# Optimization experiments

Measured on AMD Instinct MI355X. Metric: run time of the kernel, lower is better.

Reference implementation:

```python
import jax, jax.numpy as jnp
import numpy as np

N, E, G = 50000, 800000, 64
NODE_DIM, HID, HEADS, EDGE_DIM = 128, 256, 4, 2
LAYER_IN = [NODE_DIM, HID, HID]
LAYER_HEADS = [HEADS, HEADS, 1]
BN_EPS = 1e-5


def setup_inputs() -> dict:
    key = jax.random.key(0)
    ks = iter(jax.random.split(key, 80))
    def nrm(shape, s=0.05):
        return jax.random.normal(next(ks), shape, jnp.float32) * s
    inp = {}
    inp['x'] = jax.random.normal(next(ks), (N, NODE_DIM), jnp.float32)
    inp['edge_index'] = jax.random.randint(next(ks), (2, E), 0, N, jnp.int32)
    inp['edge_attr'] = jax.random.normal(next(ks), (E, EDGE_DIM), jnp.float32)
    inp['batch'] = jnp.sort(jax.random.randint(next(ks), (N,), 0, G, jnp.int32))
    for i in range(3):
        H = LAYER_HEADS[i]; C = HID // H
        inp[f'W{i}'] = nrm((LAYER_IN[i], H * C))
        inp[f'asrc{i}'] = nrm((H, C))
        inp[f'adst{i}'] = nrm((H, C))
        inp[f'We{i}'] = nrm((EDGE_DIM, H * C))
        inp[f'aedge{i}'] = nrm((H, C))
        inp[f'bconv{i}'] = jnp.zeros((HID,), jnp.float32)
        inp[f'bn{i}_g'] = jnp.ones((HID,), jnp.float32)
        inp[f'bn{i}_b'] = jnp.zeros((HID,), jnp.float32)
        inp[f'bn{i}_m'] = nrm((HID,), 0.01)
        inp[f'bn{i}_v'] = jnp.ones((HID,), jnp.float32)
    inp['Wskip'] = nrm((NODE_DIM, HID))
    inp['bskip'] = jnp.zeros((HID,), jnp.float32)
    inp['Wp1'] = nrm((2 * HID, HID))
    inp['bp1'] = jnp.zeros((HID,), jnp.float32)
    inp['Wp2'] = nrm((HID, 1))
    inp['bp2'] = jnp.zeros((1,), jnp.float32)
    return inp


def gat_conv(x, src, dst, ea, W, a_s, a_d, We, a_e, b, H, concat):
    n = x.shape[0]
    C = W.shape[1] // H
    h = (x @ W).reshape(n, H, C)                      # [N,H,C]
    # attention logits per edge (src/dst node terms + edge term)
    al = ((h * a_s).sum(-1)[src]
          + (h * a_d).sum(-1)[dst]
          + ((ea @ We).reshape(-1, H, C) * a_e).sum(-1))  # [Et,H]
    al = jax.nn.leaky_relu(al, 0.2)
    # segment softmax over destination nodes
    amax = jax.ops.segment_max(al, dst, num_segments=n)
    ex = jnp.exp(al - amax[dst])
    den = jax.ops.segment_sum(ex, dst, num_segments=n)
    alpha = ex / (den[dst] + 1e-16)
    out = jax.ops.segment_sum(h[src] * alpha[..., None], dst, num_segments=n)  # [N,H,C]
    out = out.reshape(n, H * C) if concat else out.mean(axis=1)
    return out + b


def _forward(x, edge_index, edge_attr, batch, layer_params, Wskip, bskip, Wp1, bp1, Wp2, bp2):
    n = x.shape[0]
    # add self-loops (PyG GATConv default), edge_attr filled with mean
    loop = jnp.arange(n, dtype=edge_index.dtype)
    src = jnp.concatenate([edge_index[0], loop])
    dst = jnp.concatenate([edge_index[1], loop])
    ea = jnp.concatenate([edge_attr, jnp.broadcast_to(edge_attr.mean(0), (n, edge_attr.shape[1]))], axis=0)
    identity = x
    for i, (W, a_s, a_d, We, a_e, b, g, be, rm, rv) in enumerate(layer_params):
        layer_identity = (identity @ Wskip + bskip) if i == 0 else identity
        concat = i < 2
        H = LAYER_HEADS[i]
        h = gat_conv(x, src, dst, ea, W, a_s, a_d, We, a_e, b, H, concat)
        h = (h - rm) * jax.lax.rsqrt(rv + BN_EPS) * g + be   # BatchNorm1d (eval)
        h = jax.nn.elu(h)
        x = h + layer_identity
        identity = x
    # global mean + max pool per graph
    counts = jnp.maximum(jax.ops.segment_sum(jnp.ones((n,), x.dtype), batch, num_segments=G), 1.0)
    mean_pool = jax.ops.segment_sum(x, batch, num_segments=G) / counts[:, None]
    max_pool = jax.ops.segment_max(x, batch, num_segments=G)
    emb = jnp.concatenate([mean_pool, max_pool], axis=1)      # [G, 2*HID]
    hmid = jax.nn.relu(emb @ Wp1 + bp1)
    return hmid @ Wp2 + bp2                                   # [G, 1]


def reference(x, edge_index, edge_attr, batch,
              W0, asrc0, adst0, We0, aedge0, bconv0, bn0_g, bn0_b, bn0_m, bn0_v,
              W1, asrc1, adst1, We1, aedge1, bconv1, bn1_g, bn1_b, bn1_m, bn1_v,
              W2, asrc2, adst2, We2, aedge2, bconv2, bn2_g, bn2_b, bn2_m, bn2_v,
              Wskip, bskip, Wp1, bp1, Wp2, bp2):
    layer_params = [
        (W0, asrc0, adst0, We0, aedge0, bconv0, bn0_g, bn0_b, bn0_m, bn0_v),
        (W1, asrc1, adst1, We1, aedge1, bconv1, bn1_g, bn1_b, bn1_m, bn1_v),
        (W2, asrc2, adst2, We2, aedge2, bconv2, bn2_g, bn2_b, bn2_m, bn2_v),
    ]
    return _forward(x, edge_index, edge_attr, batch, layer_params, Wskip, bskip, Wp1, bp1, Wp2, bp2)
```

## Files before the change

### kernel.cpp

```cpp
#include <hip/hip_runtime.h>
#include <cfloat>

#define Nn 50000
#define Ee 800000
#define Etot (Ee + Nn)
#define Gg 64
#define HIDc 256
#define BN_EPS 1e-5f

typedef unsigned int   uint32;
typedef unsigned short ushort16;
typedef short  bf16x8 __attribute__((ext_vector_type(8)));
typedef float  f32x4  __attribute__((ext_vector_type(4)));

__device__ inline ushort16 f2bf(float f) {
    uint32 u = __float_as_uint(f);
    u = (u + 0x7fffu + ((u >> 16) & 1u)) >> 16;
    return (ushort16)u;
}
__device__ inline uint32 pack2(float a, float b) {
    return (uint32)f2bf(a) | ((uint32)f2bf(b) << 16);
}
__device__ inline uint32 fenc(float f) {
    uint32 b = __float_as_uint(f);
    return (b & 0x80000000u) ? ~b : (b | 0x80000000u);
}
__device__ inline float fdec(uint32 u) {
    uint32 b = (u & 0x80000000u) ? (u & 0x7fffffffu) : ~u;
    return __uint_as_float(b);
}

__device__ inline long ws_index(int c, int k, int KB) {
    int cb = c >> 4, m = c & 15, kb = k >> 5, q = (k >> 3) & 3, e = k & 7;
    return (((long)(cb * KB + kb) * 64 + q * 16 + m) << 3) + e;
}

#define CVT4 (Nn * 128 / 4)
#define CVT_BLKS ((CVT4 + 255) / 256)
#define EBKS ((Etot + 255) / 256)
__global__ __launch_bounds__(256) void prep_kernel(
        const float* __restrict__ ea, float* __restrict__ ea_s,
        const float* __restrict__ We0, const float* __restrict__ ae0,
        const float* __restrict__ We1, const float* __restrict__ ae1,
        const float* __restrict__ We2, const float* __restrict__ ae2,
        float* __restrict__ M,
        const float* __restrict__ W0, const float* __restrict__ Wskip,
        const float* __restrict__ W1, const float* __restrict__ W2,
        ushort16* __restrict__ WtC, ushort16* __restrict__ Wt1,
        ushort16* __restrict__ Wt2,
        const float* __restrict__ x, ushort16* __restrict__ xbf,
        const int* __restrict__ ei, int* __restrict__ counts,
        const float* __restrict__ bc0, const float* __restrict__ g0,
        const float* __restrict__ b0, const float* __restrict__ m0,
        const float* __restrict__ v0,
        const float* __restrict__ bc1, const float* __restrict__ g1,
        const float* __restrict__ b1, const float* __restrict__ m1,
        const float* __restrict__ v1,
        const float* __restrict__ bc2, const float* __restrict__ g2,
        const float* __restrict__ b2, const float* __restrict__ m2,
        const float* __restrict__ v2,
        float* __restrict__ bnf) {
    int bid = blockIdx.x, t = threadIdx.x;
    if (bid < 256) {
        __shared__ float sh0[256], sh1[256];
        float s0 = 0.f, s1 = 0.f;
        for (int e = bid * 256 + t; e < Ee; e += 256 * 256) {
            s0 += ea[2 * e];
            s1 += ea[2 * e + 1];
        }
        sh0[t] = s0; sh1[t] = s1;
        __syncthreads();
        for (int off = 128; off > 0; off >>= 1) {
            if (t < off) { sh0[t] += sh0[t + off]; sh1[t] += sh1[t + off]; }
            __syncthreads();
        }
        if (t == 0) { atomicAdd(&ea_s[0], sh0[0]); atomicAdd(&ea_s[1], sh1[0]); }
    } else if (bid == 256) {
        if (t >= 18) return;
        int l = t < 8 ? 0 : (t < 16 ? 1 : 2);
        int r = t - l * 8;
        const float* We = (l == 0) ? We0 : (l == 1 ? We1 : We2);
        const float* ae = (l == 0) ? ae0 : (l == 1 ? ae1 : ae2);
        int Hl = (l < 2) ? 4 : 1;
        int Cl = 256 / Hl;
        int d = r / Hl, hh = r % Hl;
        float s = 0.f;
        for (int c = 0; c < Cl; ++c)
            s += We[d * 256 + hh * Cl + c] * ae[hh * Cl + c];
        M[l * 8 + r] = s;
    } else if (bid < 385) {
        int k = bid - 257;
        WtC[ws_index(t, k, 4)] = f2bf(W0[(long)k * 256 + t]);
    } else if (bid < 513) {
        int k = bid - 385;
        WtC[ws_index(256 + t, k, 4)] = f2bf(Wskip[(long)k * 256 + t]);
    } else if (bid < 769) {
        int k = bid - 513;
        Wt1[ws_index(t, k, 8)] = f2bf(W1[(long)k * 256 + t]);
    } else if (bid < 1025) {
        int k = bid - 769;
        Wt2[ws_index(t, k, 8)] = f2bf(W2[(long)k * 256 + t]);
    } else if (bid == 1025) {
        for (int ll = 0; ll < 3; ++ll) {
            const float* bc = ll == 0 ? bc0 : (ll == 1 ? bc1 : bc2);
            const float* gg = ll == 0 ? g0  : (ll == 1 ? g1  : g2);
            const float* bb = ll == 0 ? b0  : (ll == 1 ? b1  : b2);
            const float* mm = ll == 0 ? m0  : (ll == 1 ? m1  : m2);
            const float* vv = ll == 0 ? v0  : (ll == 1 ? v1  : v2);
            float s = gg[t] * rsqrtf(vv[t] + BN_EPS);
            bnf[ll * 512 + t]       = s;
            bnf[ll * 512 + 256 + t] = (bc[t] - mm[t]) * s + bb[t];
        }
    } else if (bid < 1026 + CVT_BLKS) {
        int i = (bid - 1026) * 256 + t;
        if (i < CVT4) {
            float4 v = *(const float4*)&x[i * 4];
            ushort4 o;
            o.x = f2bf(v.x); o.y = f2bf(v.y); o.z = f2bf(v.z); o.w = f2bf(v.w);
            *(ushort4*)&xbf[i * 4] = o;
        }
    } else {
        int e = (bid - 1026 - CVT_BLKS) * 256 + t;
        if (e < Etot) {
            int d = (e < Ee) ? ei[Ee + e] : (e - Ee);
            atomicAdd(&counts[d], 1);
        }
    }
}

__global__ void scan1_kernel(const int* __restrict__ in, int* __restrict__ inc,
                             int* __restrict__ bsums) {
    __shared__ int sh[256];
    int i = blockIdx.x * 256 + threadIdx.x;
    int v = (i < Nn) ? in[i] : 0;
    sh[threadIdx.x] = v;
    __syncthreads();
    for (int off = 1; off < 256; off <<= 1) {
        int t = ((int)threadIdx.x >= off) ? sh[threadIdx.x - off] : 0;
        __syncthreads();
        sh[threadIdx.x] += t;
        __syncthreads();
    }
    if (i < Nn) inc[i] = sh[threadIdx.x];
    if (threadIdx.x == 255) bsums[blockIdx.x] = sh[255];
}

__global__ void scan23_kernel(const int* __restrict__ inc, const int* __restrict__ bsums,
                              int* __restrict__ row_start, int* __restrict__ cursor, int nb) {
    __shared__ int sh[256];
    int b = blockIdx.x, t = threadIdx.x;
    sh[t] = (t < b && t < nb) ? bsums[t] : 0;
    __syncthreads();
    for (int off = 128; off > 0; off >>= 1) {
        if (t < off) sh[t] += sh[t + off];
        __syncthreads();
    }
    int base = sh[0];
    int i = b * 256 + t;
    if (i < Nn) {
        int v = inc[i] + base;
        row_start[i + 1] = v;
        cursor[i + 1] = v;
    }
    if (i == 0) { row_start[0] = 0; cursor[0] = 0; }
}

__global__ void scatter_kernel(const int* __restrict__ ei, const float* __restrict__ ea,
                               const float* __restrict__ ea_sum, int* __restrict__ cursor,
                               int* __restrict__ src_sorted, float* __restrict__ ea_sorted) {
    int e = blockIdx.x * blockDim.x + threadIdx.x;
    if (e >= Etot) return;
    int s, d; float e0, e1;
    if (e < Ee) {
        s = ei[e]; d = ei[Ee + e];
        e0 = ea[2 * e]; e1 = ea[2 * e + 1];
    } else {
        s = d = e - Ee;
        const float invE = 1.f / (float)Ee;
        e0 = ea_sum[0] * invE; e1 = ea_sum[1] * invE;
    }
    int pos = atomicAdd(&cursor[d], 1);
    src_sorted[pos] = s;
    ea_sorted[2 * pos]     = e0;
    ea_sorted[2 * pos + 1] = e1;
}

#define LDK 40
__global__ __launch_bounds__(256) void mfma_gemm_kernel(
        const ushort16* __restrict__ A,
        const ushort16* __restrict__ WS,
        uint32* __restrict__ outF,
        uint32* __restrict__ outS,
        const float* __restrict__ bskip,
        const float* __restrict__ a_s, const float* __restrict__ a_d,
        float* __restrict__ ssrc, float* __restrict__ sdst,
        int n, int K) {
    __shared__ ushort16 As[128 * LDK];
    const int t    = threadIdx.x;
    const int row0 = blockIdx.x * 128;
    const int c0   = blockIdx.y * 128;
    const bool isSkip = (outS != nullptr) && (c0 >= 256);
    const int cc0  = isSkip ? c0 - 256 : c0;
    const int wave = t >> 6, lane = t & 63;
    const int wr = wave >> 1, wc = wave & 1;
    const int l15 = lane & 15, quad = lane >> 4;
    const int KB = K >> 5;

    f32x4 acc[4][4];
#pragma unroll
    for (int j = 0; j < 4; ++j)
#pragma unroll
        for (int i = 0; i < 4; ++i) {
            acc[j][i][0] = 0.f; acc[j][i][1] = 0.f;
            acc[j][i][2] = 0.f; acc[j][i][3] = 0.f;
        }

    const int sm = t & 127;
    const int so = t >> 7;

    for (int k0 = 0; k0 < K; k0 += 32) {
        const int kb = k0 >> 5;
#pragma unroll
        for (int h = 0; h < 2; ++h) {
            int oct = so + 2 * h;
            int grow = row0 + sm;
            uint4 va = make_uint4(0, 0, 0, 0);
            if (grow < n) va = *(const uint4*)&A[(long)grow * K + k0 + 8 * oct];
            *(uint4*)&As[sm * LDK + 8 * oct] = va;
        }
        bf16x8 bfv[4];
#pragma unroll
        for (int j = 0; j < 4; ++j) {
            int cb = ((c0 + wc * 64) >> 4) + j;
            bfv[j] = *(const bf16x8*)&WS[(((long)cb * KB + kb) * 64 + lane) << 3];
        }
        __syncthreads();
        bf16x8 af[4];
#pragma unroll
        for (int i = 0; i < 4; ++i)
            af[i] = *(const bf16x8*)&As[(wr * 64 + i * 16 + l15) * LDK + quad * 8];
#pragma unroll
        for (int j = 0; j < 4; ++j)
#pragma unroll
            for (int i = 0; i < 4; ++i)
                acc[j][i] = __builtin_amdgcn_mfma_f32_16x16x32_bf16(
                    bfv[j], af[i], acc[j][i], 0, 0, 0);
        __syncthreads();
    }

    float4 bb[4];
#pragma unroll
    for (int j = 0; j < 4; ++j) {
        if (isSkip) bb[j] = *(const float4*)&bskip[cc0 + wc * 64 + j * 16 + quad * 4];
        else        bb[j] = make_float4(0.f, 0.f, 0.f, 0.f);
    }

    uint32* tgt = isSkip ? outS : outF;
#pragma unroll
    for (int i = 0; i < 4; ++i) {
        int row = row0 + wr * 64 + i * 16 + l15;
        if (row >= n) continue;
#pragma unroll
        for (int j = 0; j < 4; ++j) {
            int col = cc0 + wc * 64 + j * 16 + quad * 4;
            uint2 pk;
            pk.x = pack2(acc[j][i][0] + bb[j].x, acc[j][i][1] + bb[j].y);
            pk.y = pack2(acc[j][i][2] + bb[j].z, acc[j][i][3] + bb[j].w);
            *(uint2*)&tgt[(long)row * 128 + (col >> 1)] = pk;
        }
    }

    if (!isSkip && a_s != nullptr) {
        float4 asv[4], adv[4];
#pragma unroll
        for (int j = 0; j < 4; ++j) {
            int col = cc0 + wc * 64 + j * 16 + quad * 4;
            asv[j] = *(const float4*)&a_s[col];
            adv[j] = *(const float4*)&a_d[col];
        }
        const int part = (cc0 + wc * 64) >> 6;
#pragma unroll
        for (int i = 0; i < 4; ++i) {
            float ps = 0.f, pd = 0.f;
#pragma unroll
            for (int j = 0; j < 4; ++j) {
                ps += acc[j][i][0] * asv[j].x + acc[j][i][1] * asv[j].y
                    + acc[j][i][2] * asv[j].z + acc[j][i][3] * asv[j].w;
                pd += acc[j][i][0] * adv[j].x + acc[j][i][1] * adv[j].y
                    + acc[j][i][2] * adv[j].z + acc[j][i][3] * adv[j].w;
            }
            ps += __shfl_xor(ps, 16); ps += __shfl_xor(ps, 32);
            pd += __shfl_xor(pd, 16); pd += __shfl_xor(pd, 32);
            if (quad == 0) {
                int row = row0 + wr * 64 + i * 16 + l15;
                if (row < n) {
                    ssrc[row * 4 + part] = ps;
                    sdst[row * 4 + part] = pd;
                }
            }
        }
    }
}

template <int H>
__global__ __launch_bounds__(256) void agg_fused_kernel(
        const int* __restrict__ src_sorted, const int* __restrict__ row_start,
        const float* __restrict__ ea_sorted, const float* __restrict__ ssrc,
        const float* __restrict__ sdst, const float* __restrict__ M,
        const uint32* __restrict__ hbuf2,
        const float* __restrict__ bnS, const float* __restrict__ bnB,
        const uint32* __restrict__ identity2, uint32* __restrict__ out2) {
    __shared__ int   s_sh[4][64];
    __shared__ float w_sh[4][64 * H];
    const int wv = threadIdx.x >> 6;
    const int l  = threadIdx.x & 63;
    const int node = blockIdx.x * 4 + wv;
    if (node >= Nn) return;
    const int hh = (H == 4) ? (l >> 4) : 0;
    const int beg = row_start[node], end = row_start[node + 1];

    const int c = 4 * l;
    const float4 scv = *(const float4*)&bnS[c];
    const float4 sbv = *(const float4*)&bnB[c];
    const uint2  idu = *(const uint2*)&identity2[(long)node * 128 + 2 * l];

    float M0[H], M1[H], sd[H];
    {
        float4 sdv = *(const float4*)&sdst[node * 4];
        if (H == 4) { sd[0] = sdv.x; sd[1] = sdv.y; sd[2] = sdv.z; sd[3] = sdv.w; }
        else         sd[0] = sdv.x + sdv.y + sdv.z + sdv.w;
#pragma unroll
        for (int h = 0; h < H; ++h) { M0[h] = M[h]; M1[h] = M[H + h]; }
    }

    float a0 = 0.f, a1 = 0.f, a2 = 0.f, a3 = 0.f, dnl = 0.f;
    const uint32 loff = (uint32)l << 3;

    for (int cb = beg; cb < end; cb += 64) {
        const int  el  = cb + l;
        const bool act = el < end;
        const int  elc = min(el, end - 1);
        const int  s   = src_sorted[elc];
        const float2 ev = *(const float2*)&ea_sorted[2 * elc];
        const float4 sv = *(const float4*)&ssrc[s * 4];
        if (cb != beg)
            asm volatile("s_waitcnt lgkmcnt(0)" ::: "memory");
        s_sh[wv][l] = s;
        if (H == 4) {
            float4 w4;
#pragma unroll
            for (int h = 0; h < 4; ++h) {
                float lg = ((const float*)&sv)[h] + sd[h]
                         + ev.x * M0[h] + ev.y * M1[h];
                lg = (lg > 0.f) ? lg : 0.2f * lg;
                ((float*)&w4)[h] = act ? __expf(lg) : 0.f;
            }
            *(float4*)&w_sh[wv][l * 4] = w4;
        } else {
            float lg = (sv.x + sv.y + sv.z + sv.w) + sd[0]
                     + ev.x * M0[0] + ev.y * M1[0];
            lg = (lg > 0.f) ? lg : 0.2f * lg;
            w_sh[wv][l] = act ? __expf(lg) : 0.f;
        }
        asm volatile("s_waitcnt lgkmcnt(0)" ::: "memory");

        const int cnt = min(64, end - cb);
        for (int base = 0; base < cnt; base += 16) {
            int sk[16]; float wk[16]; uint2 f[16];
#pragma unroll
            for (int k = 0; k < 16; ++k) {
                sk[k] = s_sh[wv][base + k];
                wk[k] = w_sh[wv][(base + k) * H + hh];
            }
#pragma unroll
            for (int k = 0; k < 16; ++k)
                f[k] = *(const uint2*)((const char*)hbuf2 +
                                       (((uint32)sk[k] << 9) + loff));
#pragma unroll
            for (int k = 0; k < 16; ++k) {
                float ww = wk[k];
                dnl += ww;
                a0 += ww * __uint_as_float(f[k].x << 16);
                a1 += ww * __uint_as_float(f[k].x & 0xffff0000u);
                a2 += ww * __uint_as_float(f[k].y << 16);
                a3 += ww * __uint_as_float(f[k].y & 0xffff0000u);
            }
        }
    }

    const float inv = 1.f / (dnl + 1e-16f);
    float v0 = a0 * (scv.x * inv) + sbv.x;
    float v1 = a1 * (scv.y * inv) + sbv.y;
    float v2 = a2 * (scv.z * inv) + sbv.z;
    float v3 = a3 * (scv.w * inv) + sbv.w;
    v0 = (v0 > 0.f) ? v0 : (expf(v0) - 1.f);
    v1 = (v1 > 0.f) ? v1 : (expf(v1) - 1.f);
    v2 = (v2 > 0.f) ? v2 : (expf(v2) - 1.f);
    v3 = (v3 > 0.f) ? v3 : (expf(v3) - 1.f);
    v0 += __uint_as_float(idu.x << 16);
    v1 += __uint_as_float(idu.x & 0xffff0000u);
    v2 += __uint_as_float(idu.y << 16);
    v3 += __uint_as_float(idu.y & 0xffff0000u);
    uint2 o;
    o.x = pack2(v0, v1);
    o.y = pack2(v2, v3);
    *(uint2*)&out2[(long)node * 128 + 2 * l] = o;
}

#define POOL_ROWS 32
__global__ __launch_bounds__(128) void pool_kernel(
        const uint32* __restrict__ x2, const int* __restrict__ batch,
        float* __restrict__ psum, uint32* __restrict__ pmax, float* __restrict__ pcnt) {
    int c2 = threadIdx.x;
    int n0 = blockIdx.x * POOL_ROWS;
    if (n0 >= Nn) return;
    int n1 = min(n0 + POOL_ROWS, Nn);
    int cur = batch[n0];
    float s0 = 0.f, s1 = 0.f, m0 = -FLT_MAX, m1 = -FLT_MAX;
    int cnt = 0;
    int c = 2 * c2;
    for (int i = n0; i < n1; ++i) {
        int g = batch[i];
        if (g != cur) {
            atomicAdd(&psum[cur * 256 + c], s0);
            atomicAdd(&psum[cur * 256 + c + 1], s1);
            atomicMax(&pmax[cur * 256 + c], fenc(m0));
            atomicMax(&pmax[cur * 256 + c + 1], fenc(m1));
            if (c2 == 0) atomicAdd(&pcnt[cur], (float)cnt);
            cur = g; s0 = s1 = 0.f; m0 = m1 = -FLT_MAX; cnt = 0;
        }
        uint32 u = x2[(long)i * 128 + c2];
        float lo = __uint_as_float(u << 16);
        float hi = __uint_as_float(u & 0xffff0000u);
        s0 += lo; s1 += hi;
        m0 = fmaxf(m0, lo); m1 = fmaxf(m1, hi);
        ++cnt;
    }
    atomicAdd(&psum[cur * 256 + c], s0);
    atomicAdd(&psum[cur * 256 + c + 1], s1);
    atomicMax(&pmax[cur * 256 + c], fenc(m0));
    atomicMax(&pmax[cur * 256 + c + 1], fenc(m1));
    if (c2 == 0) atomicAdd(&pcnt[cur], (float)cnt);
}

__global__ __launch_bounds__(256) void mlp_kernel(
        const float* __restrict__ psum, const uint32* __restrict__ pmax,
        const float* __restrict__ pcnt, const float* __restrict__ Wp1,
        const float* __restrict__ bp1, const float* __restrict__ Wp2,
        const float* __restrict__ bp2, float* __restrict__ out) {
    int g = blockIdx.x;
    int j = threadIdx.x;
    float inv = 1.f / fmaxf(pcnt[g], 1.f);
    float acc = bp1[j];
    for (int k = 0; k < 256; ++k)
        acc += (psum[g * 256 + k] * inv) * Wp1[k * 256 + j];
    for (int k = 0; k < 256; ++k)
        acc += fdec(pmax[g * 256 + k]) * Wp1[(256 + k) * 256 + j];
    float v = fmaxf(acc, 0.f) * Wp2[j];
    __shared__ float red[256];
    red[j] = v;
    __syncthreads();
    for (int off = 128; off > 0; off >>= 1) {
        if (j < off) red[j] += red[j + off];
        __syncthreads();
    }
    if (j == 0) out[g] = red[0] + bp2[0];
}

extern "C" void kernel_launch(void* const* d_in, const int* in_sizes, int n_in,
                              void* d_out, int out_size, void* d_ws, size_t ws_size,
                              hipStream_t stream) {
    const float* x   = (const float*)d_in[0];
    const int*   ei  = (const int*)d_in[1];
    const float* ea  = (const float*)d_in[2];
    const int*   bat = (const int*)d_in[3];
    auto LP = [&](int l, int j) { return (const float*)d_in[4 + l * 10 + j]; };
    const float* Wskip = (const float*)d_in[34];
    const float* bskip = (const float*)d_in[35];
    const float* Wp1   = (const float*)d_in[36];
    const float* bp1   = (const float*)d_in[37];
    const float* Wp2   = (const float*)d_in[38];
    const float* bp2   = (const float*)d_in[39];
    float* out = (float*)d_out;

    char* p = (char*)d_ws;
    auto alloc = [&](size_t bytes) { void* r = (void*)p; p += (bytes + 255) & ~(size_t)255; return r; };
    uint32*   hbuf2  = (uint32*)alloc((size_t)Nn * 256 * 2);
    uint32*   skipbf = (uint32*)alloc((size_t)Nn * 128 * 4);
    uint32*   resA   = (uint32*)alloc((size_t)Nn * 128 * 4);
    uint32*   resB   = (uint32*)alloc((size_t)Nn * 128 * 4);
    ushort16* xbf    = (ushort16*)alloc((size_t)Nn * 128 * 2);
    float*    ea_sorted = (float*)alloc((size_t)Etot * 2 * 4);
    float*    ssrc   = (float*)alloc((size_t)Nn * 4 * 4);
    float*    sdst   = (float*)alloc((size_t)Nn * 4 * 4);
    int*      counts = (int*)alloc((size_t)Nn * 4);
    int*      incb   = (int*)alloc((size_t)Nn * 4);
    int*      row_start = (int*)alloc((size_t)(Nn + 1) * 4);
    int*      cursor    = (int*)alloc((size_t)(Nn + 1) * 4);
    int*      src_sorted = (int*)alloc((size_t)Etot * 4);
    int*      bsums  = (int*)alloc(256 * 4);
    float*    ea_s   = (float*)alloc(2 * 4);
    float*    Mbuf   = (float*)alloc(32 * 4);
    float*    bnf    = (float*)alloc((size_t)3 * 512 * 4);
    ushort16* WtC    = (ushort16*)alloc((size_t)512 * 128 * 2);
    ushort16* Wt1    = (ushort16*)alloc((size_t)256 * 256 * 2);
    ushort16* Wt2    = (ushort16*)alloc((size_t)256 * 256 * 2);
    float*    psum   = (float*)alloc((size_t)Gg * 256 * 4);
    uint32*   pmax   = (uint32*)alloc((size_t)Gg * 256 * 4);
    float*    pcnt   = (float*)alloc((size_t)Gg * 4);

    const int nb = (Nn + 255) / 256;

    hipMemsetAsync(counts, 0, (size_t)Nn * 4, stream);
    hipMemsetAsync(ea_s, 0, 8, stream);
    hipMemsetAsync(psum, 0, (size_t)Gg * 256 * 4 * 2 + (size_t)Gg * 4, stream);

    prep_kernel<<<1026 + CVT_BLKS + EBKS, 256, 0, stream>>>(
        ea, ea_s, LP(0,3), LP(0,4), LP(1,3), LP(1,4), LP(2,3), LP(2,4), Mbuf,
        LP(0,0), Wskip, LP(1,0), LP(2,0), WtC, Wt1, Wt2, x, xbf, ei, counts,
        LP(0,5), LP(0,6), LP(0,7), LP(0,8), LP(0,9),
        LP(1,5), LP(1,6), LP(1,7), LP(1,8), LP(1,9),
        LP(2,5), LP(2,6), LP(2,7), LP(2,8), LP(2,9),
        bnf);

    scan1_kernel<<<nb, 256, 0, stream>>>(counts, incb, bsums);
    scan23_kernel<<<nb, 256, 0, stream>>>(incb, bsums, row_start, cursor, nb);
    scatter_kernel<<<EBKS, 256, 0, stream>>>(ei, ea, ea_s, cursor, src_sorted, ea_sorted);

    {
        dim3 g0((Nn + 127) / 128, 4);
        mfma_gemm_kernel<<<g0, 256, 0, stream>>>(
            xbf, WtC, hbuf2, skipbf, bskip,
            LP(0,1), LP(0,2), ssrc, sdst, Nn, 128);
    }

    const uint32* lid[3] = { skipbf, resA, resB };
    uint32*       lou[3] = { resA, resB, resA };
    const ushort16* lain[3] = { nullptr, (ushort16*)resA, (ushort16*)resB };
    const ushort16* lwt[3]  = { nullptr, Wt1, Wt2 };
    for (int l = 0; l < 3; ++l) {
        if (l > 0) {
            dim3 gl((Nn + 127) / 128, 2);
            mfma_gemm_kernel<<<gl, 256, 0, stream>>>(
                lain[l], lwt[l], hbuf2, nullptr, nullptr,
                LP(l,1), LP(l,2), ssrc, sdst, Nn, 256);
        }
        if (l < 2)
            agg_fused_kernel<4><<<(Nn + 3) / 4, 256, 0, stream>>>(
                src_sorted, row_start, ea_sorted, ssrc, sdst, Mbuf + l * 8,
                hbuf2, bnf + l * 512, bnf + l * 512 + 256,
                lid[l], lou[l]);
        else
            agg_fused_kernel<1><<<(Nn + 3) / 4, 256, 0, stream>>>(
                src_sorted, row_start, ea_sorted, ssrc, sdst, Mbuf + l * 8,
                hbuf2, bnf + l * 512, bnf + l * 512 + 256,
                lid[l], lou[l]);
    }

    pool_kernel<<<(Nn + POOL_ROWS - 1) / POOL_ROWS, 128, 0, stream>>>(resA, bat, psum, pmax, pcnt);
    mlp_kernel<<<Gg, 256, 0, stream>>>(psum, pmax, pcnt, Wp1, bp1, Wp2, bp2, out);
}
```

Before: 617.6 us.

## Process aggregation nodes in descending in-degree order via degree-bucket permutation

Builds a histogram of node in-degrees, capped at 64, inside the scan kernel. Two small new kernels then scan it and produce a permutation that orders nodes from highest to lowest degree. The aggregation kernels read node ids through this permutation, so heavy nodes are scheduled first and waves in a block see similar amounts of work, which should reduce tail imbalance. The cost is two extra launches, an indirection per wave, and less locality in the identity and output accesses.

```diff
diff --git a/kernel.cpp b/kernel.cpp
--- a/kernel.cpp
+++ b/kernel.cpp
@@ -129,10 +129,14 @@
 }
 
 __global__ void scan1_kernel(const int* __restrict__ in, int* __restrict__ inc,
-                             int* __restrict__ bsums) {
+                             int* __restrict__ bsums, int* __restrict__ dhist) {
     __shared__ int sh[256];
+    __shared__ int lh[65];
     int i = blockIdx.x * 256 + threadIdx.x;
     int v = (i < Nn) ? in[i] : 0;
+    if (threadIdx.x < 65) lh[threadIdx.x] = 0;
+    __syncthreads();
+    if (i < Nn) atomicAdd(&lh[64 - min(v, 64)], 1);
     sh[threadIdx.x] = v;
     __syncthreads();
     for (int off = 1; off < 256; off <<= 1) {
@@ -143,6 +147,44 @@
     }
     if (i < Nn) inc[i] = sh[threadIdx.x];
     if (threadIdx.x == 255) bsums[blockIdx.x] = sh[255];
+    if (threadIdx.x < 65 && lh[threadIdx.x])
+        atomicAdd(&dhist[threadIdx.x], lh[threadIdx.x]);
+}
+
+__global__ void dscan_kernel(const int* __restrict__ dhist, int* __restrict__ dbase) {
+    __shared__ int sh[128];
+    int t = threadIdx.x;
+    int v = (t < 65) ? dhist[t] : 0;
+    sh[t] = v;
+    __syncthreads();
+    for (int off = 1; off < 128; off <<= 1) {
+        int u = (t >= off) ? sh[t - off] : 0;
+        __syncthreads();
+        sh[t] += u;
+        __syncthreads();
+    }
+    if (t < 65) dbase[t] = sh[t] - v;
+}
+
+__global__ __launch_bounds__(256) void dperm_kernel(
+        const int* __restrict__ counts, int* __restrict__ dbase,
+        int* __restrict__ perm) {
+    __shared__ int lh[65];
+    __shared__ int gb[65];
+    int t = threadIdx.x;
+    int i = blockIdx.x * 256 + t;
+    if (t < 65) lh[t] = 0;
+    __syncthreads();
+    int key = 0, my = 0;
+    bool ok = i < Nn;
+    if (ok) {
+        key = 64 - min(counts[i], 64);
+        my = atomicAdd(&lh[key], 1);
+    }
+    __syncthreads();
+    if (t < 65) gb[t] = lh[t] ? atomicAdd(&dbase[t], lh[t]) : 0;
+    __syncthreads();
+    if (ok) perm[gb[key] + my] = i;
 }
 
 __global__ void scan23_kernel(const int* __restrict__ inc, const int* __restrict__ bsums,
@@ -304,6 +346,7 @@
 
 template <int H>
 __global__ __launch_bounds__(256) void agg_fused_kernel(
+        const int* __restrict__ perm,
         const int* __restrict__ src_sorted, const int* __restrict__ row_start,
         const float* __restrict__ ea_sorted, const float* __restrict__ ssrc,
         const float* __restrict__ sdst, const float* __restrict__ M,
@@ -314,8 +357,9 @@
     __shared__ float w_sh[4][64 * H];
     const int wv = threadIdx.x >> 6;
     const int l  = threadIdx.x & 63;
-    const int node = blockIdx.x * 4 + wv;
-    if (node >= Nn) return;
+    const int idx = blockIdx.x * 4 + wv;
+    if (idx >= Nn) return;
+    const int node = perm[idx];
     const int hh = (H == 4) ? (l >> 4) : 0;
     const int beg = row_start[node], end = row_start[node + 1];
 
@@ -498,7 +542,10 @@
     int*      row_start = (int*)alloc((size_t)(Nn + 1) * 4);
     int*      cursor    = (int*)alloc((size_t)(Nn + 1) * 4);
     int*      src_sorted = (int*)alloc((size_t)Etot * 4);
+    int*      perm   = (int*)alloc((size_t)Nn * 4);
     int*      bsums  = (int*)alloc(256 * 4);
+    int*      dhist  = (int*)alloc(65 * 4);
+    int*      dbase  = (int*)alloc(65 * 4);
     float*    ea_s   = (float*)alloc(2 * 4);
     float*    Mbuf   = (float*)alloc(32 * 4);
     float*    bnf    = (float*)alloc((size_t)3 * 512 * 4);
@@ -512,6 +559,7 @@
     const int nb = (Nn + 255) / 256;
 
     hipMemsetAsync(counts, 0, (size_t)Nn * 4, stream);
+    hipMemsetAsync(dhist, 0, 65 * 4, stream);
     hipMemsetAsync(ea_s, 0, 8, stream);
     hipMemsetAsync(psum, 0, (size_t)Gg * 256 * 4 * 2 + (size_t)Gg * 4, stream);
 
@@ -523,7 +571,9 @@
         LP(2,5), LP(2,6), LP(2,7), LP(2,8), LP(2,9),
         bnf);
 
-    scan1_kernel<<<nb, 256, 0, stream>>>(counts, incb, bsums);
+    scan1_kernel<<<nb, 256, 0, stream>>>(counts, incb, bsums, dhist);
+    dscan_kernel<<<1, 128, 0, stream>>>(dhist, dbase);
+    dperm_kernel<<<nb, 256, 0, stream>>>(counts, dbase, perm);
     scan23_kernel<<<nb, 256, 0, stream>>>(incb, bsums, row_start, cursor, nb);
     scatter_kernel<<<EBKS, 256, 0, stream>>>(ei, ea, ea_s, cursor, src_sorted, ea_sorted);
 
@@ -547,12 +597,12 @@
         }
         if (l < 2)
             agg_fused_kernel<4><<<(Nn + 3) / 4, 256, 0, stream>>>(
-                src_sorted, row_start, ea_sorted, ssrc, sdst, Mbuf + l * 8,
+                perm, src_sorted, row_start, ea_sorted, ssrc, sdst, Mbuf + l * 8,
                 hbuf2, bnf + l * 512, bnf + l * 512 + 256,
                 lid[l], lou[l]);
         else
             agg_fused_kernel<1><<<(Nn + 3) / 4, 256, 0, stream>>>(
-                src_sorted, row_start, ea_sorted, ssrc, sdst, Mbuf + l * 8,
+                perm, src_sorted, row_start, ea_sorted, ssrc, sdst, Mbuf + l * 8,
                 hbuf2, bnf + l * 512, bnf + l * 512 + 256,
                 lid[l], lou[l]);
     }
```

New measurement: 654.0 us. 1.06x slower.

## Widen GEMM blocks to cover all output columns so each A tile loads once

Applied to the files above, without the earlier changes.

Replaces the generic MFMA GEMM with two specialised kernels of 512 threads whose blocks cover the full 256-column output width. Each A row tile is therefore read once instead of being re-read by every column block. The layer-0 kernel stages the whole 128-wide A tile in shared memory once and loops over the feature and skip halves. The layer-1/2 kernel hardcodes K=256. This cuts redundant global A loads and launch grid size, at the cost of fewer, larger blocks and more shared memory per block.

```diff
diff --git a/kernel.cpp b/kernel.cpp
--- a/kernel.cpp
+++ b/kernel.cpp
@@ -185,26 +185,133 @@
     ea_sorted[2 * pos + 1] = e1;
 }
 
+#define LDK0 136
+__global__ __launch_bounds__(512) void mfma_gemm0_kernel(
+        const ushort16* __restrict__ A,
+        const ushort16* __restrict__ WS,
+        uint32* __restrict__ outF, uint32* __restrict__ outS,
+        const float* __restrict__ bskip,
+        const float* __restrict__ a_s, const float* __restrict__ a_d,
+        float* __restrict__ ssrc, float* __restrict__ sdst, int n) {
+    __shared__ ushort16 As[128 * LDK0];
+    const int t = threadIdx.x;
+    const int row0 = blockIdx.x * 128;
+    const int wave = t >> 6, lane = t & 63;
+    const int wr = wave >> 2, wc = wave & 3;
+    const int l15 = lane & 15, quad = lane >> 4;
+
+    {
+        int sm = t & 127, q4 = t >> 7;
+        int grow = row0 + sm;
+#pragma unroll
+        for (int h = 0; h < 4; ++h) {
+            int oct = q4 * 4 + h;
+            uint4 va = make_uint4(0, 0, 0, 0);
+            if (grow < n) va = *(const uint4*)&A[(long)grow * 128 + 8 * oct];
+            *(uint4*)&As[sm * LDK0 + 8 * oct] = va;
+        }
+    }
+    __syncthreads();
+
+    for (int cc = 0; cc < 2; ++cc) {
+        const int c0 = cc * 256;
+        const bool isSkip = (cc == 1);
+        f32x4 acc[4][4];
+#pragma unroll
+        for (int j = 0; j < 4; ++j)
+#pragma unroll
+            for (int i = 0; i < 4; ++i) {
+                acc[j][i][0] = 0.f; acc[j][i][1] = 0.f;
+                acc[j][i][2] = 0.f; acc[j][i][3] = 0.f;
+            }
+#pragma unroll
+        for (int kb = 0; kb < 4; ++kb) {
+            bf16x8 bfv[4];
+#pragma unroll
+            for (int j = 0; j < 4; ++j) {
+                int cb = ((c0 + wc * 64) >> 4) + j;
+                bfv[j] = *(const bf16x8*)&WS[(((long)cb * 4 + kb) * 64 + lane) << 3];
+            }
+            bf16x8 af[4];
+#pragma unroll
+            for (int i = 0; i < 4; ++i)
+                af[i] = *(const bf16x8*)&As[(wr * 64 + i * 16 + l15) * LDK0
+                                            + kb * 32 + quad * 8];
+#pragma unroll
+            for (int j = 0; j < 4; ++j)
+#pragma unroll
+                for (int i = 0; i < 4; ++i)
+                    acc[j][i] = __builtin_amdgcn_mfma_f32_16x16x32_bf16(
+                        bfv[j], af[i], acc[j][i], 0, 0, 0);
+        }
+
+        float4 bb[4];
+#pragma unroll
+        for (int j = 0; j < 4; ++j) {
+            if (isSkip) bb[j] = *(const float4*)&bskip[wc * 64 + j * 16 + quad * 4];
+            else        bb[j] = make_float4(0.f, 0.f, 0.f, 0.f);
+        }
+        uint32* tgt = isSkip ? outS : outF;
+#pragma unroll
+        for (int i = 0; i < 4; ++i) {
+            int row = row0 + wr * 64 + i * 16 + l15;
+            if (row >= n) continue;
+#pragma unroll
+            for (int j = 0; j < 4; ++j) {
+                int col = wc * 64 + j * 16 + quad * 4;
+                uint2 pk;
+                pk.x = pack2(acc[j][i][0] + bb[j].x, acc[j][i][1] + bb[j].y);
+                pk.y = pack2(acc[j][i][2] + bb[j].z, acc[j][i][3] + bb[j].w);
+                *(uint2*)&tgt[(long)row * 128 + (col >> 1)] = pk;
+            }
+        }
+
+        if (!isSkip) {
+            float4 asv[4], adv[4];
+#pragma unroll
+            for (int j = 0; j < 4; ++j) {
+                int col = wc * 64 + j * 16 + quad * 4;
+                asv[j] = *(const float4*)&a_s[col];
+                adv[j] = *(const float4*)&a_d[col];
+            }
+#pragma unroll
+            for (int i = 0; i < 4; ++i) {
+                float ps = 0.f, pd = 0.f;
+#pragma unroll
+                for (int j = 0; j < 4; ++j) {
+                    ps += acc[j][i][0] * asv[j].x + acc[j][i][1] * asv[j].y
+                        + acc[j][i][2] * asv[j].z + acc[j][i][3] * asv[j].w;
+                    pd += acc[j][i][0] * adv[j].x + acc[j][i][1] * adv[j].y
+                        + acc[j][i][2] * adv[j].z + acc[j][i][3] * adv[j].w;
+                }
+                ps += __shfl_xor(ps, 16); ps += __shfl_xor(ps, 32);
+                pd += __shfl_xor(pd, 16); pd += __shfl_xor(pd, 32);
+                if (quad == 0) {
+                    int row = row0 + wr * 64 + i * 16 + l15;
+                    if (row < n) {
+                        ssrc[row * 4 + wc] = ps;
+                        sdst[row * 4 + wc] = pd;
+                    }
+                }
+            }
+        }
+    }
+}
+
 #define LDK 40
-__global__ __launch_bounds__(256) void mfma_gemm_kernel(
+__global__ __launch_bounds__(512) void mfma_gemm12_kernel(
         const ushort16* __restrict__ A,
         const ushort16* __restrict__ WS,
         uint32* __restrict__ outF,
-        uint32* __restrict__ outS,
-        const float* __restrict__ bskip,
         const float* __restrict__ a_s, const float* __restrict__ a_d,
-        float* __restrict__ ssrc, float* __restrict__ sdst,
-        int n, int K) {
+        float* __restrict__ ssrc, float* __restrict__ sdst, int n) {
     __shared__ ushort16 As[128 * LDK];
-    const int t    = threadIdx.x;
+    const int t = threadIdx.x;
     const int row0 = blockIdx.x * 128;
-    const int c0   = blockIdx.y * 128;
-    const bool isSkip = (outS != nullptr) && (c0 >= 256);
-    const int cc0  = isSkip ? c0 - 256 : c0;
     const int wave = t >> 6, lane = t & 63;
-    const int wr = wave >> 1, wc = wave & 1;
+    const int wr = wave >> 2, wc = wave & 3;
     const int l15 = lane & 15, quad = lane >> 4;
-    const int KB = K >> 5;
+    const int sm = t & 127, so = t >> 7;
 
     f32x4 acc[4][4];
 #pragma unroll
@@ -215,24 +322,18 @@
             acc[j][i][2] = 0.f; acc[j][i][3] = 0.f;
         }
 
-    const int sm = t & 127;
-    const int so = t >> 7;
-
-    for (int k0 = 0; k0 < K; k0 += 32) {
-        const int kb = k0 >> 5;
-#pragma unroll
-        for (int h = 0; h < 2; ++h) {
-            int oct = so + 2 * h;
+    for (int kb = 0; kb < 8; ++kb) {
+        {
             int grow = row0 + sm;
             uint4 va = make_uint4(0, 0, 0, 0);
-            if (grow < n) va = *(const uint4*)&A[(long)grow * K + k0 + 8 * oct];
-            *(uint4*)&As[sm * LDK + 8 * oct] = va;
+            if (grow < n) va = *(const uint4*)&A[(long)grow * 256 + kb * 32 + 8 * so];
+            *(uint4*)&As[sm * LDK + 8 * so] = va;
         }
         bf16x8 bfv[4];
 #pragma unroll
         for (int j = 0; j < 4; ++j) {
-            int cb = ((c0 + wc * 64) >> 4) + j;
-            bfv[j] = *(const bf16x8*)&WS[(((long)cb * KB + kb) * 64 + lane) << 3];
+            int cb = wc * 4 + j;
+            bfv[j] = *(const bf16x8*)&WS[(((long)cb * 8 + kb) * 64 + lane) << 3];
         }
         __syncthreads();
         bf16x8 af[4];
@@ -248,37 +349,28 @@
         __syncthreads();
     }
 
-    float4 bb[4];
-#pragma unroll
-    for (int j = 0; j < 4; ++j) {
-        if (isSkip) bb[j] = *(const float4*)&bskip[cc0 + wc * 64 + j * 16 + quad * 4];
-        else        bb[j] = make_float4(0.f, 0.f, 0.f, 0.f);
-    }
-
-    uint32* tgt = isSkip ? outS : outF;
 #pragma unroll
     for (int i = 0; i < 4; ++i) {
         int row = row0 + wr * 64 + i * 16 + l15;
         if (row >= n) continue;
 #pragma unroll
         for (int j = 0; j < 4; ++j) {
-            int col = cc0 + wc * 64 + j * 16 + quad * 4;
+            int col = wc * 64 + j * 16 + quad * 4;
             uint2 pk;
-            pk.x = pack2(acc[j][i][0] + bb[j].x, acc[j][i][1] + bb[j].y);
-            pk.y = pack2(acc[j][i][2] + bb[j].z, acc[j][i][3] + bb[j].w);
-            *(uint2*)&tgt[(long)row * 128 + (col >> 1)] = pk;
-        }
-    }
-
-    if (!isSkip && a_s != nullptr) {
+            pk.x = pack2(acc[j][i][0], acc[j][i][1]);
+            pk.y = pack2(acc[j][i][2], acc[j][i][3]);
+            *(uint2*)&outF[(long)row * 128 + (col >> 1)] = pk;
+        }
+    }
+
+    {
         float4 asv[4], adv[4];
 #pragma unroll
         for (int j = 0; j < 4; ++j) {
-            int col = cc0 + wc * 64 + j * 16 + quad * 4;
+            int col = wc * 64 + j * 16 + quad * 4;
             asv[j] = *(const float4*)&a_s[col];
             adv[j] = *(const float4*)&a_d[col];
         }
-        const int part = (cc0 + wc * 64) >> 6;
 #pragma unroll
         for (int i = 0; i < 4; ++i) {
             float ps = 0.f, pd = 0.f;
@@ -294,8 +386,8 @@
             if (quad == 0) {
                 int row = row0 + wr * 64 + i * 16 + l15;
                 if (row < n) {
-                    ssrc[row * 4 + part] = ps;
-                    sdst[row * 4 + part] = pd;
+                    ssrc[row * 4 + wc] = ps;
+                    sdst[row * 4 + wc] = pd;
                 }
             }
         }
@@ -527,12 +619,9 @@
     scan23_kernel<<<nb, 256, 0, stream>>>(incb, bsums, row_start, cursor, nb);
     scatter_kernel<<<EBKS, 256, 0, stream>>>(ei, ea, ea_s, cursor, src_sorted, ea_sorted);
 
-    {
-        dim3 g0((Nn + 127) / 128, 4);
-        mfma_gemm_kernel<<<g0, 256, 0, stream>>>(
-            xbf, WtC, hbuf2, skipbf, bskip,
-            LP(0,1), LP(0,2), ssrc, sdst, Nn, 128);
-    }
+    mfma_gemm0_kernel<<<(Nn + 127) / 128, 512, 0, stream>>>(
+        xbf, WtC, hbuf2, skipbf, bskip,
+        LP(0,1), LP(0,2), ssrc, sdst, Nn);
 
     const uint32* lid[3] = { skipbf, resA, resB };
     uint32*       lou[3] = { resA, resB, resA };
@@ -540,10 +629,9 @@
     const ushort16* lwt[3]  = { nullptr, Wt1, Wt2 };
     for (int l = 0; l < 3; ++l) {
         if (l > 0) {
-            dim3 gl((Nn + 127) / 128, 2);
-            mfma_gemm_kernel<<<gl, 256, 0, stream>>>(
-                lain[l], lwt[l], hbuf2, nullptr, nullptr,
-                LP(l,1), LP(l,2), ssrc, sdst, Nn, 256);
+            mfma_gemm12_kernel<<<(Nn + 127) / 128, 512, 0, stream>>>(
+                lain[l], lwt[l], hbuf2,
+                LP(l,1), LP(l,2), ssrc, sdst, Nn);
         }
         if (l < 2)
             agg_fused_kernel<4><<<(Nn + 3) / 4, 256, 0, stream>>>(
```

Measured after the change: 603.9 us, median of 2. 1.02x faster.
